# Kernel tuning notes

Measured on AMD Instinct MI355X. Metric: run time of the kernel, lower is better.

Reference implementation:

```python
import jax, jax.numpy as jnp
import numpy as np

N_NODE = 100000
N_EDGE = 1600000
D_FEAT = 32
DEPTH = 10
BASE_ALPHA = 1.0


def setup_inputs() -> dict:
    key = jax.random.key(0)
    k1, k2, k3, k4 = jax.random.split(key, 4)
    x = jax.random.normal(k1, (N_NODE, D_FEAT), dtype=jnp.float32)
    edge_index = jax.random.randint(k2, (2, N_EDGE), 0, N_NODE, dtype=jnp.int64)
    edge_attr = jax.random.uniform(k3, (N_EDGE,), dtype=jnp.float32)
    pe_alphas = jax.random.normal(k4, (DEPTH,), dtype=jnp.float32)
    return {"x": x, "edge_index": edge_index, "edge_attr": edge_attr, "pe_alphas": pe_alphas}


def reference(x, edge_index, edge_attr, pe_alphas):
    n = x.shape[0]
    row, col = edge_index[0], edge_index[1]
    # GCN normalization: deg from row (source of each edge), clamp isolated nodes
    deg = jax.ops.segment_sum(jnp.ones_like(edge_attr), row, num_segments=n)
    deg = jnp.where(deg < 0.5, deg + 1.0, deg)
    dinv = deg ** -0.5
    val = dinv[row] * edge_attr * dinv[col]  # [E]

    alphas = BASE_ALPHA * jnp.tanh(pe_alphas)  # [DEPTH]

    def spmm(h):  # adj @ h via gather + segment-sum scatter
        return jax.ops.segment_sum(val[:, None] * h[col], row, num_segments=n)

    # PowerConv (monomial basis): x_L = alpha_{L-1} * (adj @ x_{L-1}), x_0 = x
    def step(h, a):
        nh = a * spmm(h)
        return nh, nh

    _, ys = jax.lax.scan(step, x, alphas)  # ys: [DEPTH, n, d]
    out = jnp.concatenate([x[None], ys], axis=0)  # [DEPTH+1, n, d]
    return jnp.moveaxis(out, 0, 1)  # [n, DEPTH+1, d]
```

## Files before the change

kernel.cpp:

```cpp
#include <hip/hip_runtime.h>

#define NN 100000
#define NE 1600000
#define DF 32
#define DEPTH 10
#define LSTRIDE ((DEPTH + 1) * DF)
#define SCAN_BLOCKS 256
#define SCAN_T 256

__global__ void hist_k(const int* __restrict__ row, int* __restrict__ cnt, int e) {
    int i = blockIdx.x * blockDim.x + threadIdx.x;
    int stride = gridDim.x * blockDim.x;
    for (; i < e; i += stride) atomicAdd(&cnt[row[i]], 1);
}

__global__ void dinv_k(const int* __restrict__ cnt, float* __restrict__ dinv, int n) {
    int i = blockIdx.x * blockDim.x + threadIdx.x;
    if (i < n) {
        int c = cnt[i];
        float d = (c == 0) ? 1.0f : (float)c;
        dinv[i] = rsqrtf(d);
    }
}

__global__ void scan_partial_k(const int* __restrict__ cnt, int* __restrict__ bsum,
                               int n, int chunk) {
    __shared__ int red[SCAN_T];
    int b = blockIdx.x, t = threadIdx.x;
    int beg = b * chunk, end = min(n, beg + chunk);
    int s = 0;
    for (int i = beg + t; i < end; i += SCAN_T) s += cnt[i];
    red[t] = s;
    __syncthreads();
    for (int off = SCAN_T / 2; off; off >>= 1) {
        if (t < off) red[t] += red[t + off];
        __syncthreads();
    }
    if (t == 0) bsum[b] = red[0];
}

__global__ void scan_bsum_k(const int* __restrict__ bsum, int* __restrict__ boff) {
    __shared__ int s[SCAN_BLOCKS];
    int t = threadIdx.x;
    s[t] = bsum[t];
    __syncthreads();
    for (int off = 1; off < SCAN_BLOCKS; off <<= 1) {
        int v = (t >= off) ? s[t - off] : 0;
        __syncthreads();
        s[t] += v;
        __syncthreads();
    }
    boff[t] = (t == 0) ? 0 : s[t - 1];
}

__global__ void scan_emit_k(const int* __restrict__ cnt, const int* __restrict__ boff,
                            int* __restrict__ rowptr, int n, int chunk) {
    __shared__ int tile[SCAN_T];
    int b = blockIdx.x, t = threadIdx.x;
    int beg = b * chunk, end = min(n, beg + chunk);
    int run = boff[b];
    for (int base = beg; base < end; base += SCAN_T) {
        int i = base + t;
        int c = (i < end) ? cnt[i] : 0;
        tile[t] = c;
        __syncthreads();
        for (int off = 1; off < SCAN_T; off <<= 1) {
            int v = (t >= off) ? tile[t - off] : 0;
            __syncthreads();
            tile[t] += v;
            __syncthreads();
        }
        if (i < end) rowptr[i] = run + tile[t] - c;
        run += tile[SCAN_T - 1];
        __syncthreads();
    }
    if (b == gridDim.x - 1 && t == 0) rowptr[n] = run;
}

__global__ void scatter_k(const int* __restrict__ row, const int* __restrict__ col,
                          const float* __restrict__ ea, const float* __restrict__ dinv,
                          const int* __restrict__ rowptr, int* __restrict__ fill,
                          int2* __restrict__ cpack, int e) {
    int i = blockIdx.x * blockDim.x + threadIdx.x;
    int stride = gridDim.x * blockDim.x;
    for (; i < e; i += stride) {
        int r = row[i], c = col[i];
        float v = dinv[r] * ea[i] * dinv[c];
        int pos = rowptr[r] + atomicAdd(&fill[r], 1);
        cpack[pos] = make_int2(c, __float_as_int(v));
    }
}

__global__ void copy_k(const float* __restrict__ x, float* __restrict__ out, int n) {
    int t = blockIdx.x * blockDim.x + threadIdx.x;
    if (t < n * 8) {
        int node = t >> 3, q = t & 7;
        ((float4*)out)[(size_t)node * (LSTRIDE / 4) + q] = ((const float4*)x)[t];
    }
}

__global__ __launch_bounds__(256) void spmm_k(const int* __restrict__ rowptr,
                                              const int2* __restrict__ cpack,
                                              const float* __restrict__ pe,
                                              float* __restrict__ out, int n, int layer) {
    int gid = blockIdx.x * 8 + (threadIdx.x >> 5);
    int lane = threadIdx.x & 31;
    if (gid >= n) return;
    float alpha = tanhf(pe[layer]);
    const float* __restrict__ hsrc = out + (size_t)layer * DF + lane;
    int beg = rowptr[gid], end = rowptr[gid + 1];
    float acc = 0.f;
    int e = beg;
    for (; e + 8 <= end; e += 8) {
        int2 p[8];
#pragma unroll
        for (int u = 0; u < 8; ++u) p[u] = cpack[e + u];
        float h[8];
#pragma unroll
        for (int u = 0; u < 8; ++u) h[u] = hsrc[(size_t)p[u].x * LSTRIDE];
#pragma unroll
        for (int u = 0; u < 8; ++u) acc = fmaf(__int_as_float(p[u].y), h[u], acc);
    }
    for (; e < end; ++e) {
        int2 p = cpack[e];
        acc = fmaf(__int_as_float(p.y), hsrc[(size_t)p.x * LSTRIDE], acc);
    }
    out[(size_t)gid * LSTRIDE + (layer + 1) * DF + lane] = alpha * acc;
}

extern "C" void kernel_launch(void* const* d_in, const int* in_sizes, int n_in,
                              void* d_out, int out_size, void* d_ws, size_t ws_size,
                              hipStream_t stream) {
    const float* x  = (const float*)d_in[0];
    const int*   ei = (const int*)d_in[1];
    const float* ea = (const float*)d_in[2];
    const float* pe = (const float*)d_in[3];
    float* out = (float*)d_out;

    const int n = in_sizes[0] / DF;
    const int e = in_sizes[2];
    const int* row = ei;
    const int* col = ei + e;

    int*   cnt    = (int*)d_ws;
    int*   fill   = cnt + n;
    int*   rowptr = fill + n;
    float* dinv   = (float*)(rowptr + n + 1);
    int*   bsum   = (int*)(dinv + n);
    int*   boff   = bsum + SCAN_BLOCKS;
    size_t off = ((size_t)(boff + SCAN_BLOCKS) - (size_t)d_ws + 7) & ~(size_t)7;
    int2*  cpack = (int2*)((char*)d_ws + off);

    hipMemsetAsync(cnt, 0, (size_t)2 * n * sizeof(int), stream);

    const int chunk = (n + SCAN_BLOCKS - 1) / SCAN_BLOCKS;

    hist_k<<<2048, 256, 0, stream>>>(row, cnt, e);
    dinv_k<<<(n + 255) / 256, 256, 0, stream>>>(cnt, dinv, n);
    scan_partial_k<<<SCAN_BLOCKS, SCAN_T, 0, stream>>>(cnt, bsum, n, chunk);
    scan_bsum_k<<<1, SCAN_BLOCKS, 0, stream>>>(bsum, boff);
    scan_emit_k<<<SCAN_BLOCKS, SCAN_T, 0, stream>>>(cnt, boff, rowptr, n, chunk);
    scatter_k<<<2048, 256, 0, stream>>>(row, col, ea, dinv, rowptr, fill, cpack, e);
    copy_k<<<(n * 8 + 255) / 256, 256, 0, stream>>>(x, out, n);

    for (int L = 0; L < DEPTH; ++L) {
        spmm_k<<<(n + 7) / 8, 256, 0, stream>>>(rowptr, cpack, pe, out, n, L);
    }
}
```

Before: 597.7 us.

## Two-pass bucketed CSR build and nontemporal loads/stores in SpMM

The single atomic scatter into CSR order is replaced by two passes. First, edges are binned into 128-row buckets in a staging buffer, with the local row packed into the high bits of the column word. Second, one block per bucket sorts its edges in shared memory and writes them out contiguously, so the final CSR writes are coalesced instead of random. The SpMM loop now loads packed edges as 64-bit nontemporal loads and stores its results nontemporally to reduce cache pollution. The fixed bucket capacity of 2560 edges can overflow for skewed degree distributions, and packing the column into 17 bits limits node count to 131072.

```diff
diff --git a/kernel.cpp b/kernel.cpp
--- a/kernel.cpp
+++ b/kernel.cpp
@@ -7,6 +7,8 @@
 #define LSTRIDE ((DEPTH + 1) * DF)
 #define SCAN_BLOCKS 256
 #define SCAN_T 256
+#define RPB 128
+#define BCAP 2560
 
 __global__ void hist_k(const int* __restrict__ row, int* __restrict__ cnt, int e) {
     int i = blockIdx.x * blockDim.x + threadIdx.x;
@@ -77,18 +79,43 @@
     if (b == gridDim.x - 1 && t == 0) rowptr[n] = run;
 }
 
-__global__ void scatter_k(const int* __restrict__ row, const int* __restrict__ col,
-                          const float* __restrict__ ea, const float* __restrict__ dinv,
-                          const int* __restrict__ rowptr, int* __restrict__ fill,
-                          int2* __restrict__ cpack, int e) {
+__global__ void binA_k(const int* __restrict__ row, const int* __restrict__ col,
+                       const float* __restrict__ ea, const float* __restrict__ dinv,
+                       int* __restrict__ bfill, int2* __restrict__ stage, int e) {
     int i = blockIdx.x * blockDim.x + threadIdx.x;
     int stride = gridDim.x * blockDim.x;
     for (; i < e; i += stride) {
         int r = row[i], c = col[i];
         float v = dinv[r] * ea[i] * dinv[c];
-        int pos = rowptr[r] + atomicAdd(&fill[r], 1);
-        cpack[pos] = make_int2(c, __float_as_int(v));
-    }
+        int b = r >> 7;
+        int pos = atomicAdd(&bfill[b], 1);
+        stage[(size_t)b * BCAP + pos] =
+            make_int2((int)(((unsigned)(r & (RPB - 1)) << 17) | (unsigned)c), __float_as_int(v));
+    }
+}
+
+__global__ __launch_bounds__(256) void binB_k(const int2* __restrict__ stage,
+                                              const int* __restrict__ bfill,
+                                              const int* __restrict__ rowptr,
+                                              int2* __restrict__ cpack, int n) {
+    __shared__ int2 srt[BCAP];
+    __shared__ int lfill[RPB];
+    int b = blockIdx.x, t = threadIdx.x;
+    int r0 = b * RPB;
+    int rcount = min(RPB, n - r0);
+    for (int i = t; i < rcount; i += 256) lfill[i] = 0;
+    __syncthreads();
+    int m = bfill[b];
+    int g0 = rowptr[r0];
+    const int2* sb = stage + (size_t)b * BCAP;
+    for (int i = t; i < m; i += 256) {
+        int2 e = sb[i];
+        int rl = ((unsigned)e.x) >> 17;
+        int pos = rowptr[r0 + rl] - g0 + atomicAdd(&lfill[rl], 1);
+        srt[pos] = make_int2(e.x & 0x1FFFF, e.y);
+    }
+    __syncthreads();
+    for (int i = t; i < m; i += 256) cpack[g0 + i] = srt[i];
 }
 
 __global__ void copy_k(const float* __restrict__ x, float* __restrict__ out, int n) {
@@ -100,7 +127,7 @@
 }
 
 __global__ __launch_bounds__(256) void spmm_k(const int* __restrict__ rowptr,
-                                              const int2* __restrict__ cpack,
+                                              const unsigned long long* __restrict__ cpack,
                                               const float* __restrict__ pe,
                                               float* __restrict__ out, int n, int layer) {
     int gid = blockIdx.x * 8 + (threadIdx.x >> 5);
@@ -112,20 +139,24 @@
     float acc = 0.f;
     int e = beg;
     for (; e + 8 <= end; e += 8) {
-        int2 p[8];
+        unsigned long long p[8];
 #pragma unroll
-        for (int u = 0; u < 8; ++u) p[u] = cpack[e + u];
+        for (int u = 0; u < 8; ++u) p[u] = __builtin_nontemporal_load(&cpack[e + u]);
         float h[8];
 #pragma unroll
-        for (int u = 0; u < 8; ++u) h[u] = hsrc[(size_t)p[u].x * LSTRIDE];
+        for (int u = 0; u < 8; ++u)
+            h[u] = hsrc[(size_t)(unsigned)(p[u] & 0xFFFFFFFFu) * LSTRIDE];
 #pragma unroll
-        for (int u = 0; u < 8; ++u) acc = fmaf(__int_as_float(p[u].y), h[u], acc);
+        for (int u = 0; u < 8; ++u)
+            acc = fmaf(__uint_as_float((unsigned)(p[u] >> 32)), h[u], acc);
     }
     for (; e < end; ++e) {
-        int2 p = cpack[e];
-        acc = fmaf(__int_as_float(p.y), hsrc[(size_t)p.x * LSTRIDE], acc);
-    }
-    out[(size_t)gid * LSTRIDE + (layer + 1) * DF + lane] = alpha * acc;
+        unsigned long long p = __builtin_nontemporal_load(&cpack[e]);
+        acc = fmaf(__uint_as_float((unsigned)(p >> 32)),
+                   hsrc[(size_t)(unsigned)(p & 0xFFFFFFFFu) * LSTRIDE], acc);
+    }
+    __builtin_nontemporal_store(alpha * acc,
+                                &out[(size_t)gid * LSTRIDE + (layer + 1) * DF + lane]);
 }
 
 extern "C" void kernel_launch(void* const* d_in, const int* in_sizes, int n_in,
@@ -141,17 +172,19 @@
     const int e = in_sizes[2];
     const int* row = ei;
     const int* col = ei + e;
+    const int nbuck = (n + RPB - 1) / RPB;
 
     int*   cnt    = (int*)d_ws;
-    int*   fill   = cnt + n;
-    int*   rowptr = fill + n;
+    int*   bfill  = cnt + n;
+    int*   rowptr = bfill + nbuck;
     float* dinv   = (float*)(rowptr + n + 1);
     int*   bsum   = (int*)(dinv + n);
     int*   boff   = bsum + SCAN_BLOCKS;
-    size_t off = ((size_t)(boff + SCAN_BLOCKS) - (size_t)d_ws + 7) & ~(size_t)7;
-    int2*  cpack = (int2*)((char*)d_ws + off);
-
-    hipMemsetAsync(cnt, 0, (size_t)2 * n * sizeof(int), stream);
+    size_t off = ((size_t)(boff + SCAN_BLOCKS) - (size_t)d_ws + 15) & ~(size_t)15;
+    int2*  stage = (int2*)((char*)d_ws + off);
+    int2*  cpack = stage + (size_t)nbuck * BCAP;
+
+    hipMemsetAsync(cnt, 0, (size_t)(n + nbuck) * sizeof(int), stream);
 
     const int chunk = (n + SCAN_BLOCKS - 1) / SCAN_BLOCKS;
 
@@ -160,10 +193,12 @@
     scan_partial_k<<<SCAN_BLOCKS, SCAN_T, 0, stream>>>(cnt, bsum, n, chunk);
     scan_bsum_k<<<1, SCAN_BLOCKS, 0, stream>>>(bsum, boff);
     scan_emit_k<<<SCAN_BLOCKS, SCAN_T, 0, stream>>>(cnt, boff, rowptr, n, chunk);
-    scatter_k<<<2048, 256, 0, stream>>>(row, col, ea, dinv, rowptr, fill, cpack, e);
+    binA_k<<<2048, 256, 0, stream>>>(row, col, ea, dinv, bfill, stage, e);
+    binB_k<<<nbuck, 256, 0, stream>>>(stage, bfill, rowptr, cpack, n);
     copy_k<<<(n * 8 + 255) / 256, 256, 0, stream>>>(x, out, n);
 
     for (int L = 0; L < DEPTH; ++L) {
-        spmm_k<<<(n + 7) / 8, 256, 0, stream>>>(rowptr, cpack, pe, out, n, L);
-    }
-}
+        spmm_k<<<(n + 7) / 8, 256, 0, stream>>>(rowptr, (const unsigned long long*)cpack,
+                                                pe, out, n, L);
+    }
+}
```

After: 1.043 ms. +74.5%, slower.
